# Kernel optimization log

Hardware: AMD Instinct MI355X
Metric: run time of the kernel (lower is better)

Reference implementation:

```python
import jax, jax.numpy as jnp
from jax import lax
import numpy as np

C_IN = 64
C_OUT = 64
CQ = C_OUT // 8   # query/key channels
K = 5             # axial kernel length
RATIO = 0.7       # hybrid-norm mixing ratio
EPS = 1e-5
DN = ('NCHW', 'OIHW', 'NCHW')


def setup_inputs() -> dict:
    key = jax.random.key(0)
    ks = jax.random.split(key, 16)
    rn = lambda k, s, sc=0.05: jax.random.normal(k, s, dtype=jnp.float32) * sc
    return dict(
        x=jax.random.normal(ks[0], (4, C_IN, 256, 256), dtype=jnp.float32),
        hconv_w=rn(ks[1], (C_IN, 1, 1, K)), hconv_b=rn(ks[2], (C_IN,)),
        vconv_w=rn(ks[3], (C_IN, 1, K, 1)), vconv_b=rn(ks[4], (C_IN,)),
        pw_w=rn(ks[5], (C_OUT, C_IN)), pw_b=rn(ks[6], (C_OUT,)),
        bn_w=1.0 + rn(ks[7], (C_OUT,)), bn_b=rn(ks[8], (C_OUT,)),
        q_w=rn(ks[9], (CQ, C_OUT)), q_b=rn(ks[10], (CQ,)),
        k_w=rn(ks[11], (CQ, C_OUT)), k_b=rn(ks[12], (CQ,)),
        v_w=rn(ks[13], (C_OUT, C_OUT)), v_b=rn(ks[14], (C_OUT,)),
        gamma=rn(ks[15], (1,), 0.1),
    )


def reference(x, hconv_w, hconv_b, vconv_w, vconv_b, pw_w, pw_b,
              bn_w, bn_b, q_w, q_b, k_w, k_b, v_w, v_b, gamma):
    # ---- AxialDepthwiseConv: depthwise (1,K) + (K,1) + x, relu, pointwise ----
    h = lax.conv_general_dilated(x, hconv_w, (1, 1), [(0, 0), (K // 2, K // 2)],
                                 dimension_numbers=DN, feature_group_count=C_IN)
    h = h + hconv_b[:, None, None]
    v = lax.conv_general_dilated(x, vconv_w, (1, 1), [(K // 2, K // 2), (0, 0)],
                                 dimension_numbers=DN, feature_group_count=C_IN)
    v = v + vconv_b[:, None, None]
    a = jax.nn.relu(h + v + x)
    y = jnp.einsum('bchw,oc->bohw', a, pw_w) + pw_b[:, None, None]

    # ---- HybridNormalization: 0.7*InstanceNorm(no affine) + 0.3*BatchNorm(train) ----
    im = y.mean((2, 3), keepdims=True)
    iv = y.var((2, 3), keepdims=True)
    inn = (y - im) * lax.rsqrt(iv + EPS)
    bm = y.mean((0, 2, 3), keepdims=True)
    bv = y.var((0, 2, 3), keepdims=True)
    bnn = (y - bm) * lax.rsqrt(bv + EPS) * bn_w[:, None, None] + bn_b[:, None, None]
    y = RATIO * inn + (1.0 - RATIO) * bnn

    # ---- CrissCrossAttention ----
    q = jnp.einsum('bchw,oc->bohw', y, q_w) + q_b[:, None, None]   # (B,CQ,H,W)
    k = jnp.einsum('bchw,oc->bohw', y, k_w) + k_b[:, None, None]   # (B,CQ,H,W)
    val = jnp.einsum('bchw,oc->bohw', y, v_w) + v_b[:, None, None] # (B,C,H,W)

    # height (per column w): attn[b,w,j,i] = softmax_i( q[b,:,j,w] . k[b,:,i,w] )
    Ah = jax.nn.softmax(jnp.einsum('bcjw,bciw->bwji', q, k), axis=-1)
    # h_out[b,c,i,w] = sum_j val[b,c,j,w] * Ah[b,w,j,i]  (matches bmm(value, attn))
    h_out = jnp.einsum('bcjw,bwji->bciw', val, Ah)

    # width (per row h): attn[b,h,y,x] = softmax_x( q[b,:,h,y] . k[b,:,h,x] )
    Av = jax.nn.softmax(jnp.einsum('bchy,bchx->bhyx', q, k), axis=-1)
    v_out = jnp.einsum('bchy,bhyx->bchx', val, Av)

    out = gamma[0] * (h_out + v_out) + y

    # ---- MaxPool2d(2,2) ----
    down = lax.reduce_window(out, -jnp.inf, lax.max, (1, 1, 2, 2), (1, 1, 2, 2), 'VALID')
    return out, down
```

## Files before the change

### kernel.cpp

```cpp
#include <hip/hip_runtime.h>
#include <hip/hip_bf16.h>

#define Bn 4
#define Cc 64
#define CQn 8
#define Hh 256
#define Ww 256
#define PLANE 65536
#define LOG2E 1.4426950408889634f

typedef unsigned short ushortT;
typedef __attribute__((ext_vector_type(8))) unsigned short us8;
typedef __attribute__((ext_vector_type(4))) unsigned short us4;
typedef __attribute__((ext_vector_type(8))) __bf16 bf16x8;
typedef __attribute__((ext_vector_type(4))) float f32x4;

__device__ inline ushortT f2bf(float f) {
    __hip_bfloat16 h = __float2bfloat16(f);
    return *(ushortT*)&h;
}
__device__ inline float bf2f(ushortT u) {
    return __uint_as_float((unsigned)u << 16);
}
union BF8U { us8 u; bf16x8 b; uint4 w; };
__device__ inline us8 zero_us8() {
    BF8U z; z.w.x = 0; z.w.y = 0; z.w.z = 0; z.w.w = 0; return z.u;
}

__global__ void pack_weights_kernel(
    const float* __restrict__ pww, const float* __restrict__ qw,
    const float* __restrict__ kw, const float* __restrict__ vw,
    ushortT* __restrict__ pw_bf, ushortT* __restrict__ qk_bf,
    ushortT* __restrict__ vw_bf)
{
    int i = blockIdx.x * 256 + threadIdx.x;
    if (i < 64 * 64) pw_bf[i] = f2bf(pww[i]);
    if (i < 64 * 64) vw_bf[i] = f2bf(vw[i]);
    if (i < 8 * 64)  qk_bf[i] = f2bf(qw[i]);
    if (i >= 8 * 64 && i < 16 * 64) qk_bf[i] = f2bf(kw[i - 512]);
}

__global__ __launch_bounds__(256) void dw_kernel(
    const float* __restrict__ x,
    const float* __restrict__ hw, const float* __restrict__ hb,
    const float* __restrict__ vw, const float* __restrict__ vb,
    ushortT* __restrict__ aout)
{
    int blk = blockIdx.x;
    int bc = blk >> 4;
    int ht = blk & 15;
    int h0 = ht * 16;
    int c = bc & 63;
    int tid = threadIdx.x;
    __shared__ float rows[20][260];
    const float* xp = x + (size_t)bc * PLANE;
    #pragma unroll
    for (int i = 0; i < 20; ++i) {
        int hr = h0 - 2 + i;
        rows[i][tid + 2] = (hr >= 0 && hr < Hh) ? xp[hr * Ww + tid] : 0.f;
    }
    if (tid < 20) {
        rows[tid][0] = 0.f; rows[tid][1] = 0.f;
        rows[tid][258] = 0.f; rows[tid][259] = 0.f;
    }
    __syncthreads();

    float hw0 = hw[c * 5 + 0], hw1 = hw[c * 5 + 1], hw2 = hw[c * 5 + 2],
          hw3 = hw[c * 5 + 3], hw4 = hw[c * 5 + 4];
    float vw0 = vw[c * 5 + 0], vw1 = vw[c * 5 + 1], vw2 = vw[c * 5 + 2],
          vw3 = vw[c * 5 + 3], vw4 = vw[c * 5 + 4];
    float bias = hb[c] + vb[c];

    ushortT* op = aout + (size_t)bc * PLANE + h0 * Ww + tid;
    #pragma unroll
    for (int r = 0; r < 16; ++r) {
        float hs = hw0 * rows[r + 2][tid]     + hw1 * rows[r + 2][tid + 1]
                 + hw2 * rows[r + 2][tid + 2] + hw3 * rows[r + 2][tid + 3]
                 + hw4 * rows[r + 2][tid + 4];
        float vs = vw0 * rows[r][tid + 2]     + vw1 * rows[r + 1][tid + 2]
                 + vw2 * rows[r + 2][tid + 2] + vw3 * rows[r + 3][tid + 2]
                 + vw4 * rows[r + 4][tid + 2];
        float res = hs + vs + bias + rows[r + 2][tid + 2];
        op[r * Ww] = f2bf(fmaxf(res, 0.f));
    }
}

__global__ __launch_bounds__(256) void pw_mfma_kernel(
    const ushortT* __restrict__ a_bf, const ushortT* __restrict__ pw_bf,
    const float* __restrict__ pwb,
    float* __restrict__ y_raw, float* __restrict__ sums, float* __restrict__ sumsq)
{
    int blk = blockIdx.x;
    int b = blk >> 8;
    int t0 = (blk & 255) << 8;
    int tid = threadIdx.x, lane = tid & 63, wv = tid >> 6;
    int half = lane >> 4;
    int col = lane & 15;

    __shared__ ushortT ytile[256 * 74];

    {
        size_t base = (size_t)b * Cc * PLANE + t0 + tid;
        uint* wrow = (uint*)&ytile[tid * 74];
        #pragma unroll
        for (int c = 0; c < Cc; c += 2) {
            ushortT v0 = a_bf[base + (size_t)c * PLANE];
            ushortT v1 = a_bf[base + (size_t)(c + 1) * PLANE];
            wrow[c >> 1] = (uint)v0 | ((uint)v1 << 16);
        }
    }
    __syncthreads();

    int m0 = wv * 16;
    BF8U a0, a1;
    a0.u = *(const us8*)(pw_bf + (m0 + col) * 64 + half * 8);
    a1.u = *(const us8*)(pw_bf + (m0 + col) * 64 + 32 + half * 8);

    float bias[4], s[4], s2[4];
    #pragma unroll
    for (int r = 0; r < 4; ++r) {
        bias[r] = pwb[m0 + half * 4 + r];
        s[r] = 0.f; s2[r] = 0.f;
    }

    const uint* lw = (const uint*)ytile;
    #pragma unroll 4
    for (int t = 0; t < 16; ++t) {
        int rbase = (t * 16 + col) * 37 + half * 4;
        BF8U b0, b1;
        b0.w.x = lw[rbase];      b0.w.y = lw[rbase + 1];
        b0.w.z = lw[rbase + 2];  b0.w.w = lw[rbase + 3];
        b1.w.x = lw[rbase + 16]; b1.w.y = lw[rbase + 17];
        b1.w.z = lw[rbase + 18]; b1.w.w = lw[rbase + 19];
        f32x4 acc = (f32x4){0.f, 0.f, 0.f, 0.f};
        acc = __builtin_amdgcn_mfma_f32_16x16x32_bf16(a0.b, b0.b, acc, 0, 0, 0);
        acc = __builtin_amdgcn_mfma_f32_16x16x32_bf16(a1.b, b1.b, acc, 0, 0, 0);
        int pix = t * 16 + col;
        #pragma unroll
        for (int r = 0; r < 4; ++r) {
            int c = m0 + half * 4 + r;
            float v = acc[r] + bias[r];
            y_raw[(size_t)(b * Cc + c) * PLANE + t0 + pix] = v;
            s[r] += v; s2[r] += v * v;
        }
    }
    #pragma unroll
    for (int r = 0; r < 4; ++r) {
        #pragma unroll
        for (int d = 8; d > 0; d >>= 1) {
            s[r]  += __shfl_down(s[r], d, 16);
            s2[r] += __shfl_down(s2[r], d, 16);
        }
    }
    if (col == 0) {
        #pragma unroll
        for (int r = 0; r < 4; ++r) {
            int c = m0 + half * 4 + r;
            atomicAdd(&sums[b * Cc + c], s[r]);
            atomicAdd(&sumsq[b * Cc + c], s2[r]);
        }
    }
}

__global__ __launch_bounds__(256) void qkv_mfma_kernel(
    const float* __restrict__ y_raw,
    const float* __restrict__ sums, const float* __restrict__ sumsq,
    const float* __restrict__ bnw, const float* __restrict__ bnb,
    const ushortT* __restrict__ qk_bf, const float* __restrict__ qbias,
    const float* __restrict__ kbias,
    const ushortT* __restrict__ vw_bf, const float* __restrict__ vbias,
    ushortT* __restrict__ q, ushortT* __restrict__ k,
    ushortT* __restrict__ val)
{
    int blk = blockIdx.x;
    int b = blk >> 8;
    int t0 = (blk & 255) << 8;
    int tid = threadIdx.x, lane = tid & 63, wv = tid >> 6;
    int half = lane >> 4;
    int col = lane & 15;

    __shared__ ushortT ytile[256 * 74];
    __shared__ float alpha_s[64], beta_s[64];

    if (tid < 64) {
        int c = tid;
        float im[4], e2[4];
        float bm = 0.f, be2 = 0.f;
        #pragma unroll
        for (int bb = 0; bb < 4; ++bb) {
            im[bb] = sums[bb * Cc + c] * (1.f / 65536.f);
            e2[bb] = sumsq[bb * Cc + c] * (1.f / 65536.f);
            bm += im[bb]; be2 += e2[bb];
        }
        bm *= 0.25f; be2 *= 0.25f;
        float rsb = rsqrtf(be2 - bm * bm + 1e-5f);
        float wgt = bnw[c];
        float rsi = rsqrtf(e2[b] - im[b] * im[b] + 1e-5f);
        alpha_s[c] = 0.7f * rsi + 0.3f * rsb * wgt;
        beta_s[c]  = -0.7f * im[b] * rsi - 0.3f * bm * rsb * wgt + 0.3f * bnb[c];
    }
    __syncthreads();

    {
        size_t base = (size_t)b * Cc * PLANE + t0 + tid;
        uint* wrow = (uint*)&ytile[tid * 74];
        #pragma unroll
        for (int c = 0; c < Cc; c += 2) {
            float v0 = y_raw[base + (size_t)c * PLANE];
            float v1 = y_raw[base + (size_t)(c + 1) * PLANE];
            float n0 = alpha_s[c] * v0 + beta_s[c];
            float n1 = alpha_s[c + 1] * v1 + beta_s[c + 1];
            wrow[c >> 1] = (uint)f2bf(n0) | ((uint)f2bf(n1) << 16);
        }
    }
    __syncthreads();

    const uint* lw = (const uint*)ytile;

    {
        BF8U a0, a1;
        a0.u = *(const us8*)(qk_bf + col * 64 + half * 8);
        a1.u = *(const us8*)(qk_bf + col * 64 + 32 + half * 8);
        #pragma unroll
        for (int i = 0; i < 4; ++i) {
            int t = wv * 4 + i;
            int rbase = (t * 16 + col) * 37 + half * 4;
            BF8U b0, b1;
            b0.w.x = lw[rbase];      b0.w.y = lw[rbase + 1];
            b0.w.z = lw[rbase + 2];  b0.w.w = lw[rbase + 3];
            b1.w.x = lw[rbase + 16]; b1.w.y = lw[rbase + 17];
            b1.w.z = lw[rbase + 18]; b1.w.w = lw[rbase + 19];
            f32x4 acc = (f32x4){0.f, 0.f, 0.f, 0.f};
            acc = __builtin_amdgcn_mfma_f32_16x16x32_bf16(a0.b, b0.b, acc, 0, 0, 0);
            acc = __builtin_amdgcn_mfma_f32_16x16x32_bf16(a1.b, b1.b, acc, 0, 0, 0);
            int pix = t * 16 + col;
            #pragma unroll
            for (int r = 0; r < 4; ++r) {
                int row = half * 4 + r;
                if (row < 8)
                    q[(size_t)(b * CQn + row) * PLANE + t0 + pix] =
                        f2bf((acc[r] + qbias[row]) * LOG2E);
                else
                    k[(size_t)(b * CQn + row - 8) * PLANE + t0 + pix] = f2bf(acc[r] + kbias[row - 8]);
            }
        }
    }

    {
        int m0 = wv * 16;
        BF8U a0, a1;
        a0.u = *(const us8*)(vw_bf + (m0 + col) * 64 + half * 8);
        a1.u = *(const us8*)(vw_bf + (m0 + col) * 64 + 32 + half * 8);
        float bias[4];
        #pragma unroll
        for (int r = 0; r < 4; ++r) bias[r] = vbias[m0 + half * 4 + r];
        #pragma unroll 4
        for (int t = 0; t < 16; ++t) {
            int rbase = (t * 16 + col) * 37 + half * 4;
            BF8U b0, b1;
            b0.w.x = lw[rbase];      b0.w.y = lw[rbase + 1];
            b0.w.z = lw[rbase + 2];  b0.w.w = lw[rbase + 3];
            b1.w.x = lw[rbase + 16]; b1.w.y = lw[rbase + 17];
            b1.w.z = lw[rbase + 18]; b1.w.w = lw[rbase + 19];
            f32x4 acc = (f32x4){0.f, 0.f, 0.f, 0.f};
            acc = __builtin_amdgcn_mfma_f32_16x16x32_bf16(a0.b, b0.b, acc, 0, 0, 0);
            acc = __builtin_amdgcn_mfma_f32_16x16x32_bf16(a1.b, b1.b, acc, 0, 0, 0);
            int pix = t * 16 + col;
            #pragma unroll
            for (int r = 0; r < 4; ++r) {
                int c = m0 + half * 4 + r;
                val[(size_t)(b * Cc + c) * PLANE + t0 + pix] = f2bf(acc[r] + bias[r]);
            }
        }
    }
}

__global__ __launch_bounds__(256) void transpose_all_kernel(
    const ushortT* __restrict__ qb, ushortT* __restrict__ qT,
    const ushortT* __restrict__ kb, ushortT* __restrict__ kT,
    const ushortT* __restrict__ vb, ushortT* __restrict__ vT)
{
    int blk = blockIdx.x;
    int plane = blk >> 6;
    int tile = blk & 63;
    const ushortT* src; ushortT* dst;
    if (plane < 32)      { src = qb + (size_t)plane * PLANE;        dst = qT + (size_t)plane * PLANE; }
    else if (plane < 64) { src = kb + (size_t)(plane - 32) * PLANE; dst = kT + (size_t)(plane - 32) * PLANE; }
    else                 { src = vb + (size_t)(plane - 64) * PLANE; dst = vT + (size_t)(plane - 64) * PLANE; }
    int th = (tile >> 3) * 32;
    int tw = (tile & 7) * 32;
    __shared__ ushortT t[32][34];
    int lw = threadIdx.x & 31;
    int lh = threadIdx.x >> 5;
    #pragma unroll
    for (int i = 0; i < 4; ++i)
        t[lh + 8 * i][lw] = src[(th + lh + 8 * i) * Ww + tw + lw];
    __syncthreads();
    #pragma unroll
    for (int i = 0; i < 4; ++i)
        dst[(tw + lh + 8 * i) * Hh + th + lw] = t[lw][lh + 8 * i];
}

__global__ __launch_bounds__(256) void attn_kernel(
    const ushortT* __restrict__ q0, const ushortT* __restrict__ k0,
    const ushortT* __restrict__ v0, ushortT* __restrict__ o0,
    const ushortT* __restrict__ q1, const ushortT* __restrict__ k1,
    const ushortT* __restrict__ v1, ushortT* __restrict__ o1)
{
    int blk = blockIdx.x;
    int sel = blk >> 10;
    const ushortT* __restrict__ q   = sel ? q1 : q0;
    const ushortT* __restrict__ k   = sel ? k1 : k0;
    const ushortT* __restrict__ val = sel ? v1 : v0;
    ushortT* __restrict__ outp      = sel ? o1 : o0;
    int bblk = blk & 1023;
    int b = bblk >> 8;
    int r = bblk & 255;
    int tid = threadIdx.x;
    int lane = tid & 63;
    int wv = tid >> 6;
    int col = lane & 15;
    int quad = lane >> 4;

    __shared__ ushortT q_s[256 * 8];
    __shared__ ushortT k_s[256 * 8];
    __shared__ ushortT A_lds[4 * 256 * 8];
    __shared__ float mhat[256];
    __shared__ float kred[32];
    __shared__ float lsum[4][32];

    size_t vbase = (size_t)b * Cc * PLANE + (size_t)r * Ww
                 + (size_t)(wv * 16 + col) * PLANE + quad * 8;
    BF8U afb[2];
    afb[0].u = *(const us8*)(val + vbase);

    size_t qkbase = (size_t)b * CQn * PLANE + (size_t)r * Ww + tid;
    float qf[8], ka[8];
    {
        BF8U qp, kp;
        #pragma unroll
        for (int c = 0; c < 8; ++c) {
            ushortT qv = q[qkbase + (size_t)c * PLANE];
            ushortT kv = k[qkbase + (size_t)c * PLANE];
            qp.u[c] = qv; kp.u[c] = kv;
            qf[c] = bf2f(qv);
            ka[c] = fabsf(bf2f(kv));
        }
        *(us8*)&q_s[tid * 8] = qp.u;
        *(us8*)&k_s[tid * 8] = kp.u;
    }
    #pragma unroll
    for (int d = 1; d < 64; d <<= 1)
        #pragma unroll
        for (int c = 0; c < 8; ++c)
            ka[c] = fmaxf(ka[c], __shfl_xor(ka[c], d));
    if (lane == 0)
        #pragma unroll
        for (int c = 0; c < 8; ++c) kred[wv * 8 + c] = ka[c];
    __syncthreads();

    {
        float mh = 0.f;
        #pragma unroll
        for (int c = 0; c < 8; ++c) {
            float km = fmaxf(fmaxf(kred[c], kred[8 + c]),
                             fmaxf(kred[16 + c], kred[24 + c]));
            mh += fabsf(qf[c]) * km;
        }
        mhat[tid] = mh;
    }
    __syncthreads();

    BF8U kc[4];
    #pragma unroll
    for (int i = 0; i < 4; ++i)
        kc[i].u = *(const us8*)&k_s[((wv * 4 + i) * 16 + col) * 8];
    f32x4 acc[16];
    #pragma unroll
    for (int t = 0; t < 16; ++t) acc[t] = (f32x4){0.f, 0.f, 0.f, 0.f};

    #pragma unroll
    for (int ks = 0; ks < 8; ++ks) {
        if (ks < 7)
            afb[(ks + 1) & 1].u = *(const us8*)(val + vbase + (ks + 1) * 32);
        float ps[8];
        #pragma unroll
        for (int e = 0; e < 8; ++e) ps[e] = 0.f;
        #pragma unroll
        for (int jj2 = 0; jj2 < 2; ++jj2) {
            int jt = ks * 2 + jj2;
            BF8U qa; qa.u = zero_us8();
            if (quad == 0) qa.u = *(const us8*)&q_s[(jt * 16 + col) * 8];
            float mh4[4];
            #pragma unroll
            for (int rr = 0; rr < 4; ++rr) mh4[rr] = mhat[jt * 16 + quad * 4 + rr];
            #pragma unroll
            for (int i = 0; i < 4; ++i) {
                f32x4 sacc = (f32x4){0.f, 0.f, 0.f, 0.f};
                sacc = __builtin_amdgcn_mfma_f32_16x16x32_bf16(qa.b, kc[i].b, sacc, 0, 0, 0);
                us4 pk;
                #pragma unroll
                for (int rr = 0; rr < 4; ++rr) {
                    float e = __builtin_amdgcn_exp2f(sacc[rr] - mh4[rr]);
                    ps[jj2 * 4 + rr] += e;
                    pk[rr] = f2bf(e);
                }
                int irow = (wv * 4 + i) * 16 + col;
                int jq = jj2 * 2 + (quad >> 1);
                *(us4*)&A_lds[(jq * 256 + irow) * 8 + (quad & 1) * 4] = pk;
            }
        }
        #pragma unroll
        for (int d = 1; d < 16; d <<= 1)
            #pragma unroll
            for (int e = 0; e < 8; ++e)
                ps[e] += __shfl_xor(ps[e], d);
        if (col == 0) {
            #pragma unroll
            for (int jj2 = 0; jj2 < 2; ++jj2)
                #pragma unroll
                for (int rr = 0; rr < 4; ++rr)
                    lsum[wv][jj2 * 16 + quad * 4 + rr] = ps[jj2 * 4 + rr];
        }
        __syncthreads();
        f32x4 l0 = *(const f32x4*)&lsum[0][quad * 8];
        f32x4 l1 = *(const f32x4*)&lsum[0][quad * 8 + 4];
        #pragma unroll
        for (int w = 1; w < 4; ++w) {
            l0 += *(const f32x4*)&lsum[w][quad * 8];
            l1 += *(const f32x4*)&lsum[w][quad * 8 + 4];
        }
        BF8U av;
        #pragma unroll
        for (int e = 0; e < 4; ++e) {
            av.u[e]     = f2bf(bf2f(afb[ks & 1].u[e])     * __builtin_amdgcn_rcpf(l0[e]));
            av.u[4 + e] = f2bf(bf2f(afb[ks & 1].u[4 + e]) * __builtin_amdgcn_rcpf(l1[e]));
        }
        #pragma unroll
        for (int t = 0; t < 16; ++t) {
            BF8U bfr;
            bfr.u = *(const us8*)&A_lds[(quad * 256 + t * 16 + col) * 8];
            acc[t] = __builtin_amdgcn_mfma_f32_16x16x32_bf16(av.b, bfr.b, acc[t], 0, 0, 0);
        }
        __syncthreads();
    }

    size_t obase = (size_t)b * Cc * PLANE + (size_t)r * Ww;
    #pragma unroll
    for (int t = 0; t < 16; ++t) {
        int i = t * 16 + col;
        #pragma unroll
        for (int rr = 0; rr < 4; ++rr) {
            int c = wv * 16 + quad * 4 + rr;
            outp[obase + (size_t)c * PLANE + i] = f2bf(acc[t][rr]);
        }
    }
}

__global__ __launch_bounds__(256) void final_kernel(
    const ushortT* __restrict__ houtT, const ushortT* __restrict__ hout0,
    const float* __restrict__ y_raw,
    const float* __restrict__ sums, const float* __restrict__ sumsq,
    const float* __restrict__ bnw, const float* __restrict__ bnb,
    const float* __restrict__ gamma,
    float* __restrict__ out, float* __restrict__ down)
{
    int blk = blockIdx.x;
    int tile = blk & 63;
    int bc = blk >> 6;
    int b = bc >> 6;
    int c = bc & 63;
    int th = (tile >> 3) * 32;
    int tw = (tile & 7) * 32;

    float im[4], e2[4];
    float bm = 0.f, be2 = 0.f;
    #pragma unroll
    for (int bb = 0; bb < 4; ++bb) {
        im[bb] = sums[bb * Cc + c] * (1.f / 65536.f);
        e2[bb] = sumsq[bb * Cc + c] * (1.f / 65536.f);
        bm += im[bb]; be2 += e2[bb];
    }
    bm *= 0.25f; be2 *= 0.25f;
    float rsb = rsqrtf(be2 - bm * bm + 1e-5f);
    float wgt = bnw[c];
    float rsi = rsqrtf(e2[b] - im[b] * im[b] + 1e-5f);
    float al = 0.7f * rsi + 0.3f * rsb * wgt;
    float bt = -0.7f * im[b] * rsi - 0.3f * bm * rsb * wgt + 0.3f * bnb[c];

    __shared__ float t[32][33];
    const ushortT* hT = houtT + (size_t)bc * PLANE;
    {
        int ww = threadIdx.x >> 3;
        int hh = (threadIdx.x & 7) * 4;
        us4 v4 = *(const us4*)(hT + (size_t)(tw + ww) * Hh + th + hh);
        t[hh + 0][ww] = __uint_as_float((unsigned)v4[0] << 16);
        t[hh + 1][ww] = __uint_as_float((unsigned)v4[1] << 16);
        t[hh + 2][ww] = __uint_as_float((unsigned)v4[2] << 16);
        t[hh + 3][ww] = __uint_as_float((unsigned)v4[3] << 16);
    }
    __syncthreads();
    float g = gamma[0];
    int qw_ = threadIdx.x & 15;
    int qh_ = threadIdx.x >> 4;
    const float* yb = y_raw + (size_t)bc * PLANE;
    const ushortT* hb = hout0 + (size_t)bc * PLANE;
    float* ob = out + (size_t)bc * PLANE;
    float mx = -1e30f;
    float2 res[2];
    #pragma unroll
    for (int i = 0; i < 2; ++i) {
        int hh = 2 * qh_ + i;
        int off = (th + hh) * Ww + tw + 2 * qw_;
        uint hv = *(const uint*)(hb + off);
        float2 y = *(const float2*)(yb + off);
        float y0 = al * y.x + bt;
        float y1 = al * y.y + bt;
        float o0 = g * (t[hh][2 * qw_]     + bf2f((ushortT)(hv & 0xffff))) + y0;
        float o1 = g * (t[hh][2 * qw_ + 1] + bf2f((ushortT)(hv >> 16)))   + y1;
        res[i] = make_float2(o0, o1);
        mx = fmaxf(mx, fmaxf(o0, o1));
    }
    #pragma unroll
    for (int i = 0; i < 2; ++i) {
        int off = (th + 2 * qh_ + i) * Ww + tw + 2 * qw_;
        *(float2*)(ob + off) = res[i];
    }
    down[(size_t)bc * 16384 + (th / 2 + qh_) * 128 + tw / 2 + qw_] = mx;
}

extern "C" void kernel_launch(void* const* d_in, const int* in_sizes, int n_in,
                              void* d_out, int out_size, void* d_ws, size_t ws_size,
                              hipStream_t stream)
{
    const float* x     = (const float*)d_in[0];
    const float* hw    = (const float*)d_in[1];
    const float* hb    = (const float*)d_in[2];
    const float* vw    = (const float*)d_in[3];
    const float* vb    = (const float*)d_in[4];
    const float* pww   = (const float*)d_in[5];
    const float* pwb   = (const float*)d_in[6];
    const float* bnw   = (const float*)d_in[7];
    const float* bnb   = (const float*)d_in[8];
    const float* qw    = (const float*)d_in[9];
    const float* qb    = (const float*)d_in[10];
    const float* kw    = (const float*)d_in[11];
    const float* kb    = (const float*)d_in[12];
    const float* vw2   = (const float*)d_in[13];
    const float* vb2   = (const float*)d_in[14];
    const float* gamma = (const float*)d_in[15];

    float* ws = (float*)d_ws;
    const size_t NP = (size_t)Bn * Cc * PLANE;
    const size_t NQ = (size_t)Bn * CQn * PLANE;
    float* y_raw  = ws;
    float* slotB  = ws + NP;
    float* slotC  = ws + 2 * NP;
    float* slotD  = ws + 2 * NP + NP / 2;
    float* ptr    = ws + 3 * NP;
    ushortT* qbuf = (ushortT*)ptr;
    ushortT* kbuf = qbuf + NQ;
    ushortT* qT   = kbuf + NQ;
    ushortT* kT   = qT + NQ;
    float* sums   = (float*)(kT + NQ);
    float* sumsq  = sums + 256;
    ushortT* pw_bf = (ushortT*)(sumsq + 256);
    ushortT* qk_bf = pw_bf + 64 * 64;
    ushortT* vw_bf = qk_bf + 16 * 64;

    ushortT* a_buf = (ushortT*)slotC;
    ushortT* valT  = (ushortT*)slotC;
    ushortT* valb  = (ushortT*)slotD;
    ushortT* hout0 = (ushortT*)slotB;
    ushortT* houtT = hout0 + NP;
    float* out  = (float*)d_out;
    float* down = out + NP;

    hipMemsetAsync(sums, 0, 512 * sizeof(float), stream);
    pack_weights_kernel<<<dim3(16), dim3(256), 0, stream>>>(
        pww, qw, kw, vw2, pw_bf, qk_bf, vw_bf);
    dw_kernel<<<dim3(Bn * Cc * 16), dim3(256), 0, stream>>>(
        x, hw, hb, vw, vb, a_buf);
    pw_mfma_kernel<<<dim3(Bn * 256), dim3(256), 0, stream>>>(
        a_buf, pw_bf, pwb, y_raw, sums, sumsq);
    qkv_mfma_kernel<<<dim3(Bn * 256), dim3(256), 0, stream>>>(
        y_raw, sums, sumsq, bnw, bnb, qk_bf, qb, kb, vw_bf, vb2,
        qbuf, kbuf, valb);
    transpose_all_kernel<<<dim3(320 * 64), dim3(256), 0, stream>>>(
        qbuf, qT, kbuf, kT, valb, valT);
    attn_kernel<<<dim3(2 * Bn * Hh), dim3(256), 0, stream>>>(
        qbuf, kbuf, valb, hout0, qT, kT, valT, houtT);
    final_kernel<<<dim3(Bn * Cc * 64), dim3(256), 0, stream>>>(
        houtT, hout0, y_raw, sums, sumsq, bnw, bnb, gamma, out, down);
}
```

Baseline: 370.8 us.

## Double-buffer attention tiles and row sums to overlap slab compute with MFMA

New measurement: 369.8 us. Within noise of the previous version (-0.3%).

```diff
diff --git a/kernel.cpp b/kernel.cpp
--- a/kernel.cpp
+++ b/kernel.cpp
@@ -324,10 +324,10 @@
 
     __shared__ ushortT q_s[256 * 8];
     __shared__ ushortT k_s[256 * 8];
-    __shared__ ushortT A_lds[4 * 256 * 8];
+    __shared__ ushortT A_lds[2][4 * 256 * 8];
     __shared__ float mhat[256];
     __shared__ float kred[32];
-    __shared__ float lsum[4][32];
+    __shared__ float lsum[2][4][32];
 
     size_t vbase = (size_t)b * Cc * PLANE + (size_t)r * Ww
                  + (size_t)(wv * 16 + col) * PLANE + quad * 8;
@@ -379,16 +379,13 @@
     #pragma unroll
     for (int t = 0; t < 16; ++t) acc[t] = (f32x4){0.f, 0.f, 0.f, 0.f};
 
-    #pragma unroll
-    for (int ks = 0; ks < 8; ++ks) {
-        if (ks < 7)
-            afb[(ks + 1) & 1].u = *(const us8*)(val + vbase + (ks + 1) * 32);
+    auto compute_slab = [&](int kslab, int buf) {
         float ps[8];
         #pragma unroll
         for (int e = 0; e < 8; ++e) ps[e] = 0.f;
         #pragma unroll
         for (int jj2 = 0; jj2 < 2; ++jj2) {
-            int jt = ks * 2 + jj2;
+            int jt = kslab * 2 + jj2;
             BF8U qa; qa.u = zero_us8();
             if (quad == 0) qa.u = *(const us8*)&q_s[(jt * 16 + col) * 8];
             float mh4[4];
@@ -407,7 +404,7 @@
                 }
                 int irow = (wv * 4 + i) * 16 + col;
                 int jq = jj2 * 2 + (quad >> 1);
-                *(us4*)&A_lds[(jq * 256 + irow) * 8 + (quad & 1) * 4] = pk;
+                *(us4*)&A_lds[buf][(jq * 256 + irow) * 8 + (quad & 1) * 4] = pk;
             }
         }
         #pragma unroll
@@ -420,26 +417,37 @@
             for (int jj2 = 0; jj2 < 2; ++jj2)
                 #pragma unroll
                 for (int rr = 0; rr < 4; ++rr)
-                    lsum[wv][jj2 * 16 + quad * 4 + rr] = ps[jj2 * 4 + rr];
-        }
-        __syncthreads();
-        f32x4 l0 = *(const f32x4*)&lsum[0][quad * 8];
-        f32x4 l1 = *(const f32x4*)&lsum[0][quad * 8 + 4];
+                    lsum[buf][wv][jj2 * 16 + quad * 4 + rr] = ps[jj2 * 4 + rr];
+        }
+    };
+
+    compute_slab(0, 0);
+    __syncthreads();
+
+    #pragma unroll
+    for (int ks = 0; ks < 8; ++ks) {
+        int cur = ks & 1;
+        if (ks < 7) {
+            afb[cur ^ 1].u = *(const us8*)(val + vbase + (ks + 1) * 32);
+            compute_slab(ks + 1, cur ^ 1);
+        }
+        f32x4 l0 = *(const f32x4*)&lsum[cur][0][quad * 8];
+        f32x4 l1 = *(const f32x4*)&lsum[cur][0][quad * 8 + 4];
         #pragma unroll
         for (int w = 1; w < 4; ++w) {
-            l0 += *(const f32x4*)&lsum[w][quad * 8];
-            l1 += *(const f32x4*)&lsum[w][quad * 8 + 4];
+            l0 += *(const f32x4*)&lsum[cur][w][quad * 8];
+            l1 += *(const f32x4*)&lsum[cur][w][quad * 8 + 4];
         }
         BF8U av;
         #pragma unroll
         for (int e = 0; e < 4; ++e) {
-            av.u[e]     = f2bf(bf2f(afb[ks & 1].u[e])     * __builtin_amdgcn_rcpf(l0[e]));
-            av.u[4 + e] = f2bf(bf2f(afb[ks & 1].u[4 + e]) * __builtin_amdgcn_rcpf(l1[e]));
+            av.u[e]     = f2bf(bf2f(afb[cur].u[e])     * __builtin_amdgcn_rcpf(l0[e]));
+            av.u[4 + e] = f2bf(bf2f(afb[cur].u[4 + e]) * __builtin_amdgcn_rcpf(l1[e]));
         }
         #pragma unroll
         for (int t = 0; t < 16; ++t) {
             BF8U bfr;
-            bfr.u = *(const us8*)&A_lds[(quad * 256 + t * 16 + col) * 8];
+            bfr.u = *(const us8*)&A_lds[cur][(quad * 256 + t * 16 + col) * 8];
             acc[t] = __builtin_amdgcn_mfma_f32_16x16x32_bf16(av.b, bfr.b, acc[t], 0, 0, 0);
         }
         __syncthreads();
```
